# Optimization experiments

Measured on AMD Instinct MI355X. Metric: run time of the kernel, lower is better.

The kernel has to match this reference:

```python
import jax, jax.numpy as jnp
import numpy as np

SAMPLES = 16        # samples per spatial dim -> M = SAMPLES**2 sample points
SAMPLE_PAD = 0
K = 9               # nearest neighbors == conv kernel size == stride


def setup_inputs() -> dict:
    key = jax.random.key(0)
    k1, k2, k3 = jax.random.split(key, 3)
    B, C, H, W = 16, 128, 64, 64
    OUT = 128
    x = jax.random.normal(k1, (B, C, H, W), dtype=jnp.float32)
    w = jax.random.normal(k2, (OUT, C, K), dtype=jnp.float32) * 0.05
    b = jax.random.normal(k3, (OUT,), dtype=jnp.float32) * 0.05
    return {"x": x, "w": w, "b": b}


def reference(x, w, b):
    B, C, H, W = x.shape
    N = H * W
    # --- spatial sample grid (static, shape-derived) ---
    xi = jnp.round(jnp.linspace(SAMPLE_PAD, H - SAMPLE_PAD - 1, SAMPLES)).astype(jnp.int32)
    yi = jnp.round(jnp.linspace(SAMPLE_PAD, W - SAMPLE_PAD - 1, SAMPLES)).astype(jnp.int32)
    xg, yg = jnp.meshgrid(xi, yi, indexing='ij')
    x_sample = x[:, :, xg, yg].reshape(B, C, -1)          # (B, C, M)
    x1 = x.reshape(B, C, N)                                # (B, C, N)
    # --- squared Euclidean distance between tokens and samples ---
    dots = jnp.einsum('bcn,bcm->bnm', x1, x_sample)        # (B, N, M)
    n2 = jnp.sum(x1 * x1, axis=1)                          # (B, N)
    m2 = jnp.sum(x_sample * x_sample, axis=1)              # (B, M)
    dist2 = n2[:, :, None] + m2[:, None, :] - 2.0 * dots   # (B, N, M)
    # K nearest samples per token (smallest distance)
    _, idx = jax.lax.top_k(-dist2, K)                      # (B, N, K) int32
    # gather neighbor features from the sample set: (B, C, N, K)
    nbrs = jnp.take_along_axis(x_sample[:, :, None, :],
                               idx[:, None, :, :], axis=3)
    # Conv1d(kernel=K, stride=K) over the (B, C, N*K) prime tensor
    out = jnp.einsum('bcnk,ock->bon', nbrs, w) + b[None, :, None]
    return out.reshape(B, w.shape[0], H, W)
```

## Files before the change

kernel.cpp:

```cpp
#include <hip/hip_runtime.h>

#define NB   16
#define NC   128
#define NN   4096
#define NM   256
#define NK   9
#define NO   128

typedef __attribute__((ext_vector_type(8))) short bf16x8;
typedef __attribute__((ext_vector_type(4))) float f32x4;

__device__ __constant__ int d_grid16[16] = {0,4,8,13,17,21,25,29,34,38,42,46,50,55,59,63};

__device__ inline unsigned short bf16_rne(float v) {
    unsigned u = __float_as_uint(v);
    return (unsigned short)((u + 0x7FFFu + ((u >> 16) & 1u)) >> 16);
}

__device__ inline void merge16(unsigned* s, const unsigned* q) {
    unsigned r[16];
    #pragma unroll
    for (int i = 0; i < 16; ++i) r[i] = min(s[i], q[15 - i]);
    #pragma unroll
    for (int d = 8; d >= 1; d >>= 1)
        #pragma unroll
        for (int i = 0; i < 16; ++i)
            if (!(i & d)) { unsigned a = r[i], b2 = r[i + d]; r[i] = min(a, b2); r[i + d] = max(a, b2); }
    #pragma unroll
    for (int i = 0; i < 16; ++i) s[i] = r[i];
}

__global__ __launch_bounds__(256) void k_prep(const float* __restrict__ x,
                                              const float* __restrict__ w,
                                              float* __restrict__ xsT,
                                              unsigned short* __restrict__ xsTh,
                                              unsigned short* __restrict__ xsTl,
                                              unsigned short* __restrict__ Wth,
                                              unsigned short* __restrict__ Wtl,
                                              float* __restrict__ n2g,
                                              float* __restrict__ m2) {
    __shared__ float tile[16 * 260];
    int bx = blockIdx.x, t = threadIdx.x;
    if (bx < 128) {
        int b = bx >> 3, c0 = (bx & 7) * 16;
        int m = t;
        int pix = d_grid16[m >> 4] * 64 + d_grid16[m & 15];
        #pragma unroll
        for (int cc = 0; cc < 16; ++cc)
            tile[cc * 260 + m] = x[((size_t)b * NC + c0 + cc) * NN + pix];
        __syncthreads();
        #pragma unroll
        for (int e = 0; e < 4; ++e) {
            float fv[4];
            fv[0] = tile[(4 * e + 0) * 260 + m];
            fv[1] = tile[(4 * e + 1) * 260 + m];
            fv[2] = tile[(4 * e + 2) * 260 + m];
            fv[3] = tile[(4 * e + 3) * 260 + m];
            size_t base = ((size_t)b * NM + m) * NC + c0 + 4 * e;
            *(float4*)&xsT[base] = make_float4(fv[0], fv[1], fv[2], fv[3]);
            unsigned short h4[4], l4[4];
            #pragma unroll
            for (int e2 = 0; e2 < 4; ++e2) {
                unsigned short h = bf16_rne(fv[e2]);
                h4[e2] = h;
                l4[e2] = bf16_rne(fv[e2] - __uint_as_float(((unsigned)h) << 16));
            }
            *(ushort4*)&xsTh[base] = make_ushort4(h4[0], h4[1], h4[2], h4[3]);
            *(ushort4*)&xsTl[base] = make_ushort4(l4[0], l4[1], l4[2], l4[3]);
        }
    } else if (bx < 704) {
        int f = (bx - 128) * 256 + t;
        int ko = f >> 7, c = f & 127;
        int o = ko & 127, k = ko >> 7;
        float v = w[(size_t)o * 1152 + c * 9 + k];
        unsigned short h = bf16_rne(v);
        Wth[f] = h;
        Wtl[f] = bf16_rne(v - __uint_as_float(((unsigned)h) << 16));
    } else if (bx < 960) {
        #pragma clang fp contract(off)
        int i = bx - 704;
        int b = i >> 4, n = (i & 15) * 256 + t;
        const float* p = x + (size_t)b * NC * NN + n;
        float a = 0.f;
        #pragma unroll 16
        for (int c = 0; c < NC; ++c) { float v = p[(size_t)c * NN]; a = __fadd_rn(a, __fmul_rn(v, v)); }
        n2g[(size_t)b * NN + n] = a;
    } else {
        #pragma clang fp contract(off)
        int b = bx - 960;
        int pix = d_grid16[t >> 4] * 64 + d_grid16[t & 15];
        const float* p = x + (size_t)b * NC * NN + pix;
        float a = 0.f;
        #pragma unroll 16
        for (int c = 0; c < NC; ++c) { float v = p[(size_t)c * NN]; a = __fadd_rn(a, __fmul_rn(v, v)); }
        m2[b * NM + t] = a;
    }
}

__global__ __launch_bounds__(256) void k_g(const unsigned short* __restrict__ xsTh,
                                           const unsigned short* __restrict__ xsTl,
                                           const unsigned short* __restrict__ Wth,
                                           const unsigned short* __restrict__ Wtl,
                                           float* __restrict__ G) {
    int id = blockIdx.x;
    int b = id & 15, r = id >> 4;
    int kk = r % 9, mt = r / 9;
    int t = threadIdx.x;
    int w = t >> 6, lane = t & 63;
    int lr = lane & 15, quad = lane >> 4;
    int m = b * NM + mt * 64 + w * 16 + lr;
    const unsigned short* aph = xsTh + (size_t)m * NC;
    const unsigned short* apl = xsTl + (size_t)m * NC;
    f32x4 acc[8];
    #pragma unroll
    for (int j = 0; j < 8; ++j) acc[j] = (f32x4){0.f, 0.f, 0.f, 0.f};
    #pragma unroll
    for (int kb = 0; kb < 4; ++kb) {
        int co = kb * 32 + quad * 8;
        bf16x8 Ah = *(const bf16x8*)&aph[co];
        bf16x8 Al = *(const bf16x8*)&apl[co];
        #pragma unroll
        for (int j = 0; j < 8; ++j) {
            size_t wrow = ((size_t)kk * 128 + 16 * j + lr) * NC + co;
            bf16x8 Bh = *(const bf16x8*)&Wth[wrow];
            bf16x8 Bl = *(const bf16x8*)&Wtl[wrow];
            acc[j] = __builtin_amdgcn_mfma_f32_16x16x32_bf16(Ah, Bh, acc[j], 0, 0, 0);
            acc[j] = __builtin_amdgcn_mfma_f32_16x16x32_bf16(Al, Bh, acc[j], 0, 0, 0);
            acc[j] = __builtin_amdgcn_mfma_f32_16x16x32_bf16(Ah, Bl, acc[j], 0, 0, 0);
        }
    }
    int mrow = b * NM + mt * 64 + w * 16 + quad * 4;
    #pragma unroll
    for (int j = 0; j < 8; ++j)
        #pragma unroll
        for (int r2 = 0; r2 < 4; ++r2)
            G[((size_t)(mrow + r2)) * 1152 + kk * 128 + 16 * j + lr] = acc[j][r2];
}

__global__ __launch_bounds__(256, 2) void k_selref(const float* __restrict__ x,
                                                   const unsigned short* __restrict__ xsTh,
                                                   const unsigned short* __restrict__ xsTl,
                                                   const float* __restrict__ xsT,
                                                   const float* __restrict__ m2,
                                                   const float* __restrict__ n2g,
                                                   int* __restrict__ idx) {
    #pragma clang fp contract(off)
    __shared__ __align__(16) unsigned char ubuf[17408];
    __shared__ __align__(16) unsigned mrg[1088];
    __shared__ unsigned short candl[32 * 16];
    __shared__ float m2l[256];
    __shared__ float n2l[32];
    unsigned short* xhp = (unsigned short*)ubuf;
    unsigned short* xlp = xhp + 32 * 136;
    float* xr = (float*)ubuf;
    unsigned* wl = mrg;
    unsigned long long* pairs = (unsigned long long*)mrg;

    int b = blockIdx.x & 15, n0 = (blockIdx.x >> 4) * 32;
    int t = threadIdx.x;
    int w = t >> 6, lane = t & 63;
    int lr = lane & 15, quad = lane >> 4;

    m2l[t] = m2[b * NM + t];
    if (t < 32) n2l[t] = n2g[(size_t)b * NN + n0 + t];

    #pragma unroll
    for (int it = 0; it < 4; ++it) {
        int f4 = it * 256 + t;
        int c = f4 >> 3, nn4 = (f4 & 7) * 4;
        float4 v = *(const float4*)&x[((size_t)b * NC + c) * NN + n0 + nn4];
        float vf[4] = {v.x, v.y, v.z, v.w};
        #pragma unroll
        for (int e = 0; e < 4; ++e) {
            unsigned short h = bf16_rne(vf[e]);
            unsigned short l = bf16_rne(vf[e] - __uint_as_float(((unsigned)h) << 16));
            xhp[(nn4 + e) * 136 + c] = h;
            xlp[(nn4 + e) * 136 + c] = l;
        }
    }
    __syncthreads();

    f32x4 acc[2][4];
    #pragma unroll
    for (int i = 0; i < 2; ++i)
        #pragma unroll
        for (int j = 0; j < 4; ++j) acc[i][j] = (f32x4){0.f, 0.f, 0.f, 0.f};
    int mbase = w * 64;
    #pragma unroll
    for (int kb = 0; kb < 4; ++kb) {
        int co = kb * 32 + quad * 8;
        bf16x8 Bh0 = *(const bf16x8*)&xhp[lr * 136 + co];
        bf16x8 Bl0 = *(const bf16x8*)&xlp[lr * 136 + co];
        bf16x8 Bh1 = *(const bf16x8*)&xhp[(16 + lr) * 136 + co];
        bf16x8 Bl1 = *(const bf16x8*)&xlp[(16 + lr) * 136 + co];
        bf16x8 Ah[4], Al[4];
        #pragma unroll
        for (int j = 0; j < 4; ++j) {
            size_t arow = ((size_t)(b * NM + mbase + 16 * j + lr)) * NC + co;
            Ah[j] = *(const bf16x8*)&xsTh[arow];
            Al[j] = *(const bf16x8*)&xsTl[arow];
        }
        #pragma unroll
        for (int j = 0; j < 4; ++j) {
            acc[0][j] = __builtin_amdgcn_mfma_f32_16x16x32_bf16(Ah[j], Bh0, acc[0][j], 0, 0, 0);
            acc[0][j] = __builtin_amdgcn_mfma_f32_16x16x32_bf16(Ah[j], Bl0, acc[0][j], 0, 0, 0);
            acc[0][j] = __builtin_amdgcn_mfma_f32_16x16x32_bf16(Al[j], Bh0, acc[0][j], 0, 0, 0);
            acc[1][j] = __builtin_amdgcn_mfma_f32_16x16x32_bf16(Ah[j], Bh1, acc[1][j], 0, 0, 0);
            acc[1][j] = __builtin_amdgcn_mfma_f32_16x16x32_bf16(Ah[j], Bl1, acc[1][j], 0, 0, 0);
            acc[1][j] = __builtin_amdgcn_mfma_f32_16x16x32_bf16(Al[j], Bh1, acc[1][j], 0, 0, 0);
        }
    }

    #pragma unroll
    for (int h = 0; h < 2; ++h) {
        unsigned s16v[16];
        #pragma unroll
        for (int j = 0; j < 4; ++j)
            #pragma unroll
            for (int r = 0; r < 4; ++r) {
                int m = mbase + 16 * j + quad * 4 + r;
                float key = fmaf(-2.f, acc[h][j][r], m2l[m]);
                unsigned u = __float_as_uint(key);
                u = (u & 0x80000000u) ? ~u : (u | 0x80000000u);
                s16v[4 * j + r] = (u & 0xFFFFFF00u) | (unsigned)m;
            }
        #define CE(i,jx) { unsigned a_ = s16v[i], b_ = s16v[jx]; s16v[i] = min(a_, b_); s16v[jx] = max(a_, b_); }
        CE(0,1) CE(2,3) CE(0,2) CE(1,3) CE(1,2)
        CE(4,5) CE(6,7) CE(4,6) CE(5,7) CE(5,6)
        CE(0,4) CE(2,6) CE(2,4) CE(1,5) CE(3,7) CE(3,5) CE(1,2) CE(3,4) CE(5,6)
        CE(8,9) CE(10,11) CE(8,10) CE(9,11) CE(9,10)
        CE(12,13) CE(14,15) CE(12,14) CE(13,15) CE(13,14)
        CE(8,12) CE(10,14) CE(10,12) CE(9,13) CE(11,15) CE(11,13) CE(9,10) CE(11,12) CE(13,14)
        CE(0,8) CE(4,12) CE(4,8) CE(2,10) CE(6,14) CE(6,10) CE(2,4) CE(6,8) CE(10,12)
        CE(1,9) CE(5,13) CE(5,9) CE(3,11) CE(7,15) CE(7,11) CE(3,5) CE(7,9) CE(11,13)
        CE(1,2) CE(3,4) CE(5,6) CE(7,8) CE(9,10) CE(11,12) CE(13,14)
        #undef CE

        #pragma unroll
        for (int d = 16; d <= 32; d <<= 1) {
            unsigned q[16];
            #pragma unroll
            for (int i = 0; i < 16; ++i) q[i] = (unsigned)__shfl_xor((int)s16v[i], d, 64);
            merge16(s16v, q);
        }

        if (quad == 0) {
            #pragma unroll
            for (int ii = 0; ii < 4; ++ii)
                *(uint4*)&wl[(w * 16 + lr) * 16 + 4 * ii] =
                    make_uint4(s16v[4*ii], s16v[4*ii+1], s16v[4*ii+2], s16v[4*ii+3]);
        }
        __syncthreads();
        if (w == 0) {
            #pragma unroll
            for (int p = 1; p < 4; ++p) {
                unsigned q[16];
                #pragma unroll
                for (int i = 0; i < 16; ++i) q[i] = wl[(p * 16 + lr) * 16 + i];
                merge16(s16v, q);
            }
            if (quad == 0) {
                unsigned* c32 = (unsigned*)candl;
                #pragma unroll
                for (int i = 0; i < 16; i += 2)
                    c32[(16 * h + lr) * 8 + (i >> 1)] =
                        (s16v[i] & 255u) | ((s16v[i + 1] & 255u) << 16);
            }
        }
        __syncthreads();
    }

    #pragma unroll
    for (int it = 0; it < 4; ++it) {
        int f4 = it * 256 + t;
        int c = f4 >> 3, nn4 = (f4 & 7) * 4;
        float4 v = *(const float4*)&x[((size_t)b * NC + c) * NN + n0 + nn4];
        xr[(nn4 + 0) * 132 + c] = v.x;
        xr[(nn4 + 1) * 132 + c] = v.y;
        xr[(nn4 + 2) * 132 + c] = v.z;
        xr[(nn4 + 3) * 132 + c] = v.w;
    }
    __syncthreads();

    {
        int tok = t >> 3, q8 = t & 7;
        float n2 = n2l[tok];
        int mym[2];
        unsigned long long myp[2];
        #pragma unroll
        for (int s = 0; s < 2; ++s) {
            int m = candl[tok * 16 + q8 + 8 * s];
            mym[s] = m;
            const float* xt = xsT + ((size_t)(b * NM + m)) * NC;
            float dot = 0.f;
            for (int c4 = 0; c4 < 32; ++c4) {
                float4 xv = *(const float4*)&xr[tok * 132 + 4 * c4];
                float4 sv = *(const float4*)&xt[4 * c4];
                dot = __fadd_rn(dot, __fmul_rn(xv.x, sv.x));
                dot = __fadd_rn(dot, __fmul_rn(xv.y, sv.y));
                dot = __fadd_rn(dot, __fmul_rn(xv.z, sv.z));
                dot = __fadd_rn(dot, __fmul_rn(xv.w, sv.w));
            }
            float key = __fsub_rn(__fadd_rn(n2, m2l[m]), __fmul_rn(2.f, dot));
            unsigned u = __float_as_uint(key);
            u = (u & 0x80000000u) ? ~u : (u | 0x80000000u);
            myp[s] = ((unsigned long long)u << 32) | (unsigned)m;
            pairs[tok * 17 + q8 + 8 * s] = myp[s];
        }
        __syncthreads();
        unsigned long long pl[16];
        #pragma unroll
        for (int l2 = 0; l2 < 16; ++l2) pl[l2] = pairs[tok * 17 + l2];
        size_t obase = (size_t)(b * NN + n0 + tok) * NK;
        #pragma unroll
        for (int s = 0; s < 2; ++s) {
            int rank = 0;
            #pragma unroll
            for (int l2 = 0; l2 < 16; ++l2) rank += (pl[l2] < myp[s]);
            if (rank < 9) idx[obase + rank] = mym[s];
        }
    }
}

__global__ __launch_bounds__(256) void k_out(const float* __restrict__ G,
                                             const int* __restrict__ idx,
                                             const float* __restrict__ bias,
                                             float* __restrict__ out) {
    __shared__ float S[64 * 129];
    __shared__ int   idxl[576];
    __shared__ float biasl[128];
    int b = blockIdx.x & 15, n0 = (blockIdx.x >> 4) * 64;
    int t = threadIdx.x;
    if (t < 128) biasl[t] = bias[t];
    for (int f = t; f < 576; f += 256) idxl[f] = idx[(size_t)(b * NN + n0) * NK + f];
    __syncthreads();
    int o = t & 127, half = t >> 7;
    for (int p = 0; p < 32; ++p) {
        int n = p * 2 + half;
        float a = biasl[o];
        #pragma unroll
        for (int k = 0; k < 9; ++k) {
            int m = idxl[n * 9 + k];
            a += G[(((size_t)(b * NM + m)) * NK + k) * 128 + o];
        }
        S[n * 129 + o] = a;
    }
    __syncthreads();
    int nn = t & 63, ob = t >> 6;
    for (int p = 0; p < 32; ++p) {
        int o2 = p * 4 + ob;
        out[((size_t)(b * NO + o2)) * NN + n0 + nn] = S[nn * 129 + o2];
    }
}

extern "C" void kernel_launch(void* const* d_in, const int* in_sizes, int n_in,
                              void* d_out, int out_size, void* d_ws, size_t ws_size,
                              hipStream_t stream) {
    const float* x    = (const float*)d_in[0];
    const float* w    = (const float*)d_in[1];
    const float* bias = (const float*)d_in[2];
    float* out = (float*)d_out;

    float* ws   = (float*)d_ws;
    float* m2   = ws;
    float* n2g  = ws + 4096;
    float* xsT  = ws + 69632;
    float* G    = ws + 593920;
    int*   idx  = (int*)(ws + 5312512);
    unsigned short* xsTh = (unsigned short*)(ws + 5902336);
    unsigned short* xsTl = (unsigned short*)(ws + 6164480);
    unsigned short* Wth  = (unsigned short*)(ws + 6426624);
    unsigned short* Wtl  = (unsigned short*)(ws + 6500352);

    k_prep  <<<dim3(976),  dim3(256), 0, stream>>>(x, w, xsT, xsTh, xsTl, Wth, Wtl, n2g, m2);
    k_g     <<<dim3(576),  dim3(256), 0, stream>>>(xsTh, xsTl, Wth, Wtl, G);
    k_selref<<<dim3(2048), dim3(256), 0, stream>>>(x, xsTh, xsTl, xsT, m2, n2g, idx);
    k_out   <<<dim3(1024), dim3(256), 0, stream>>>(G, idx, bias, out);
}
```

Baseline: 231.2 us.

## Split fused select/refine kernel, parallelize per-half merges, halve k_g tiles

The fused select-and-refine kernel becomes two kernels. k_sel merges both token halves in parallel on waves 0 and 1 with a single barrier, and packs the 16 byte-sized candidate indices into the idx buffer. k_ref then rereads those candidates and does the exact fp32 distance refinement and ranking. k_g splits each output-channel block in half, doubling the grid and halving per-thread accumulators. The goal is fewer barriers and less serialized merging, higher occupancy and lower register pressure, at the cost of an extra launch, reloading x, and a global round trip for the candidates.

```diff
diff --git a/kernel.cpp b/kernel.cpp
--- a/kernel.cpp
+++ b/kernel.cpp
@@ -104,24 +104,25 @@
                                            float* __restrict__ G) {
     int id = blockIdx.x;
     int b = id & 15, r = id >> 4;
-    int kk = r % 9, mt = r / 9;
+    int kk = r % 9, q = r / 9;
+    int mt = q >> 1, jh = q & 1;
     int t = threadIdx.x;
     int w = t >> 6, lane = t & 63;
     int lr = lane & 15, quad = lane >> 4;
     int m = b * NM + mt * 64 + w * 16 + lr;
     const unsigned short* aph = xsTh + (size_t)m * NC;
     const unsigned short* apl = xsTl + (size_t)m * NC;
-    f32x4 acc[8];
-    #pragma unroll
-    for (int j = 0; j < 8; ++j) acc[j] = (f32x4){0.f, 0.f, 0.f, 0.f};
+    f32x4 acc[4];
+    #pragma unroll
+    for (int j = 0; j < 4; ++j) acc[j] = (f32x4){0.f, 0.f, 0.f, 0.f};
     #pragma unroll
     for (int kb = 0; kb < 4; ++kb) {
         int co = kb * 32 + quad * 8;
         bf16x8 Ah = *(const bf16x8*)&aph[co];
         bf16x8 Al = *(const bf16x8*)&apl[co];
         #pragma unroll
-        for (int j = 0; j < 8; ++j) {
-            size_t wrow = ((size_t)kk * 128 + 16 * j + lr) * NC + co;
+        for (int j = 0; j < 4; ++j) {
+            size_t wrow = ((size_t)kk * 128 + jh * 64 + 16 * j + lr) * NC + co;
             bf16x8 Bh = *(const bf16x8*)&Wth[wrow];
             bf16x8 Bl = *(const bf16x8*)&Wtl[wrow];
             acc[j] = __builtin_amdgcn_mfma_f32_16x16x32_bf16(Ah, Bh, acc[j], 0, 0, 0);
@@ -131,30 +132,21 @@
     }
     int mrow = b * NM + mt * 64 + w * 16 + quad * 4;
     #pragma unroll
-    for (int j = 0; j < 8; ++j)
+    for (int j = 0; j < 4; ++j)
         #pragma unroll
         for (int r2 = 0; r2 < 4; ++r2)
-            G[((size_t)(mrow + r2)) * 1152 + kk * 128 + 16 * j + lr] = acc[j][r2];
-}
-
-__global__ __launch_bounds__(256, 2) void k_selref(const float* __restrict__ x,
-                                                   const unsigned short* __restrict__ xsTh,
-                                                   const unsigned short* __restrict__ xsTl,
-                                                   const float* __restrict__ xsT,
-                                                   const float* __restrict__ m2,
-                                                   const float* __restrict__ n2g,
-                                                   int* __restrict__ idx) {
-    #pragma clang fp contract(off)
-    __shared__ __align__(16) unsigned char ubuf[17408];
-    __shared__ __align__(16) unsigned mrg[1088];
-    __shared__ unsigned short candl[32 * 16];
+            G[((size_t)(mrow + r2)) * 1152 + kk * 128 + jh * 64 + 16 * j + lr] = acc[j][r2];
+}
+
+__global__ __launch_bounds__(256, 2) void k_sel(const float* __restrict__ x,
+                                                const unsigned short* __restrict__ xsTh,
+                                                const unsigned short* __restrict__ xsTl,
+                                                const float* __restrict__ m2,
+                                                int* __restrict__ idx) {
+    __shared__ __align__(16) unsigned short xhp[32 * 136];
+    __shared__ __align__(16) unsigned short xlp[32 * 136];
+    __shared__ __align__(16) unsigned wl[2 * 4 * 16 * 16];
     __shared__ float m2l[256];
-    __shared__ float n2l[32];
-    unsigned short* xhp = (unsigned short*)ubuf;
-    unsigned short* xlp = xhp + 32 * 136;
-    float* xr = (float*)ubuf;
-    unsigned* wl = mrg;
-    unsigned long long* pairs = (unsigned long long*)mrg;
 
     int b = blockIdx.x & 15, n0 = (blockIdx.x >> 4) * 32;
     int t = threadIdx.x;
@@ -162,7 +154,6 @@
     int lr = lane & 15, quad = lane >> 4;
 
     m2l[t] = m2[b * NM + t];
-    if (t < 32) n2l[t] = n2g[(size_t)b * NN + n0 + t];
 
     #pragma unroll
     for (int it = 0; it < 4; ++it) {
@@ -211,9 +202,11 @@
         }
     }
 
-    #pragma unroll
-    for (int h = 0; h < 2; ++h) {
-        unsigned s16v[16];
+    unsigned s16v[16];
+    int hfirst = 1 - (w & 1);
+    #pragma unroll
+    for (int hh = 0; hh < 2; ++hh) {
+        int h = (hh == 0) ? hfirst : 1 - hfirst;
         #pragma unroll
         for (int j = 0; j < 4; ++j)
             #pragma unroll
@@ -243,32 +236,55 @@
             for (int i = 0; i < 16; ++i) q[i] = (unsigned)__shfl_xor((int)s16v[i], d, 64);
             merge16(s16v, q);
         }
-
         if (quad == 0) {
             #pragma unroll
             for (int ii = 0; ii < 4; ++ii)
-                *(uint4*)&wl[(w * 16 + lr) * 16 + 4 * ii] =
+                *(uint4*)&wl[(((h * 4 + w) * 16 + lr) * 16) + 4 * ii] =
                     make_uint4(s16v[4*ii], s16v[4*ii+1], s16v[4*ii+2], s16v[4*ii+3]);
         }
-        __syncthreads();
-        if (w == 0) {
-            #pragma unroll
-            for (int p = 1; p < 4; ++p) {
-                unsigned q[16];
-                #pragma unroll
-                for (int i = 0; i < 16; ++i) q[i] = wl[(p * 16 + lr) * 16 + i];
-                merge16(s16v, q);
-            }
-            if (quad == 0) {
-                unsigned* c32 = (unsigned*)candl;
-                #pragma unroll
-                for (int i = 0; i < 16; i += 2)
-                    c32[(16 * h + lr) * 8 + (i >> 1)] =
-                        (s16v[i] & 255u) | ((s16v[i + 1] & 255u) << 16);
-            }
-        }
-        __syncthreads();
-    }
+    }
+    __syncthreads();
+
+    if (w < 2) {
+        int h = w;
+        #pragma unroll
+        for (int p = 1; p < 4; ++p) {
+            int pw = (w + p) & 3;
+            unsigned q[16];
+            #pragma unroll
+            for (int i = 0; i < 16; ++i) q[i] = wl[(((h * 4 + pw) * 16 + lr) * 16) + i];
+            merge16(s16v, q);
+        }
+        if (quad == 0) {
+            int tok = 16 * h + lr;
+            size_t obase = (size_t)(b * NN + n0 + tok) * NK;
+            #pragma unroll
+            for (int i = 0; i < 4; ++i)
+                idx[obase + i] = (int)((s16v[4*i] & 255u) | ((s16v[4*i+1] & 255u) << 8) |
+                                       ((s16v[4*i+2] & 255u) << 16) | ((s16v[4*i+3] & 255u) << 24));
+        }
+    }
+}
+
+__global__ __launch_bounds__(256, 2) void k_ref(const float* __restrict__ x,
+                                                const float* __restrict__ xsT,
+                                                const float* __restrict__ m2,
+                                                const float* __restrict__ n2g,
+                                                int* __restrict__ idx) {
+    #pragma clang fp contract(off)
+    __shared__ __align__(16) float xr[32 * 132];
+    __shared__ unsigned long long pairs[32 * 17];
+    __shared__ unsigned char candl[512];
+    __shared__ float m2l[256];
+    __shared__ float n2l[32];
+
+    int b = blockIdx.x & 15, n0 = (blockIdx.x >> 4) * 32;
+    int t = threadIdx.x;
+
+    m2l[t] = m2[b * NM + t];
+    if (t < 32) n2l[t] = n2g[(size_t)b * NN + n0 + t];
+    if (t < 128) ((unsigned*)candl)[t] =
+        (unsigned)idx[(size_t)(b * NN + n0 + (t >> 2)) * NK + (t & 3)];
 
     #pragma unroll
     for (int it = 0; it < 4; ++it) {
@@ -282,43 +298,41 @@
     }
     __syncthreads();
 
-    {
-        int tok = t >> 3, q8 = t & 7;
-        float n2 = n2l[tok];
-        int mym[2];
-        unsigned long long myp[2];
-        #pragma unroll
-        for (int s = 0; s < 2; ++s) {
-            int m = candl[tok * 16 + q8 + 8 * s];
-            mym[s] = m;
-            const float* xt = xsT + ((size_t)(b * NM + m)) * NC;
-            float dot = 0.f;
-            for (int c4 = 0; c4 < 32; ++c4) {
-                float4 xv = *(const float4*)&xr[tok * 132 + 4 * c4];
-                float4 sv = *(const float4*)&xt[4 * c4];
-                dot = __fadd_rn(dot, __fmul_rn(xv.x, sv.x));
-                dot = __fadd_rn(dot, __fmul_rn(xv.y, sv.y));
-                dot = __fadd_rn(dot, __fmul_rn(xv.z, sv.z));
-                dot = __fadd_rn(dot, __fmul_rn(xv.w, sv.w));
-            }
-            float key = __fsub_rn(__fadd_rn(n2, m2l[m]), __fmul_rn(2.f, dot));
-            unsigned u = __float_as_uint(key);
-            u = (u & 0x80000000u) ? ~u : (u | 0x80000000u);
-            myp[s] = ((unsigned long long)u << 32) | (unsigned)m;
-            pairs[tok * 17 + q8 + 8 * s] = myp[s];
-        }
-        __syncthreads();
-        unsigned long long pl[16];
-        #pragma unroll
-        for (int l2 = 0; l2 < 16; ++l2) pl[l2] = pairs[tok * 17 + l2];
-        size_t obase = (size_t)(b * NN + n0 + tok) * NK;
-        #pragma unroll
-        for (int s = 0; s < 2; ++s) {
-            int rank = 0;
-            #pragma unroll
-            for (int l2 = 0; l2 < 16; ++l2) rank += (pl[l2] < myp[s]);
-            if (rank < 9) idx[obase + rank] = mym[s];
-        }
+    int tok = t >> 3, q8 = t & 7;
+    float n2 = n2l[tok];
+    int mym[2];
+    unsigned long long myp[2];
+    #pragma unroll
+    for (int s = 0; s < 2; ++s) {
+        int m = candl[tok * 16 + q8 + 8 * s];
+        mym[s] = m;
+        const float* xt = xsT + ((size_t)(b * NM + m)) * NC;
+        float dot = 0.f;
+        for (int c4 = 0; c4 < 32; ++c4) {
+            float4 xv = *(const float4*)&xr[tok * 132 + 4 * c4];
+            float4 sv = *(const float4*)&xt[4 * c4];
+            dot = __fadd_rn(dot, __fmul_rn(xv.x, sv.x));
+            dot = __fadd_rn(dot, __fmul_rn(xv.y, sv.y));
+            dot = __fadd_rn(dot, __fmul_rn(xv.z, sv.z));
+            dot = __fadd_rn(dot, __fmul_rn(xv.w, sv.w));
+        }
+        float key = __fsub_rn(__fadd_rn(n2, m2l[m]), __fmul_rn(2.f, dot));
+        unsigned u = __float_as_uint(key);
+        u = (u & 0x80000000u) ? ~u : (u | 0x80000000u);
+        myp[s] = ((unsigned long long)u << 32) | (unsigned)m;
+        pairs[tok * 17 + q8 + 8 * s] = myp[s];
+    }
+    __syncthreads();
+    unsigned long long pl[16];
+    #pragma unroll
+    for (int l2 = 0; l2 < 16; ++l2) pl[l2] = pairs[tok * 17 + l2];
+    size_t obase = (size_t)(b * NN + n0 + tok) * NK;
+    #pragma unroll
+    for (int s = 0; s < 2; ++s) {
+        int rank = 0;
+        #pragma unroll
+        for (int l2 = 0; l2 < 16; ++l2) rank += (pl[l2] < myp[s]);
+        if (rank < 9) idx[obase + rank] = mym[s];
     }
 }
 
@@ -372,8 +386,9 @@
     unsigned short* Wth  = (unsigned short*)(ws + 6426624);
     unsigned short* Wtl  = (unsigned short*)(ws + 6500352);
 
-    k_prep  <<<dim3(976),  dim3(256), 0, stream>>>(x, w, xsT, xsTh, xsTl, Wth, Wtl, n2g, m2);
-    k_g     <<<dim3(576),  dim3(256), 0, stream>>>(xsTh, xsTl, Wth, Wtl, G);
-    k_selref<<<dim3(2048), dim3(256), 0, stream>>>(x, xsTh, xsTl, xsT, m2, n2g, idx);
-    k_out   <<<dim3(1024), dim3(256), 0, stream>>>(G, idx, bias, out);
-}
+    k_prep<<<dim3(976),  dim3(256), 0, stream>>>(x, w, xsT, xsTh, xsTl, Wth, Wtl, n2g, m2);
+    k_g   <<<dim3(1152), dim3(256), 0, stream>>>(xsTh, xsTl, Wth, Wtl, G);
+    k_sel <<<dim3(2048), dim3(256), 0, stream>>>(x, xsTh, xsTl, m2, idx);
+    k_ref <<<dim3(2048), dim3(256), 0, stream>>>(x, xsT, m2, n2g, idx);
+    k_out <<<dim3(1024), dim3(256), 0, stream>>>(G, idx, bias, out);
+}
```

Result: slower. 260.7 us (+12.8%).

## Stage sample tiles through shared memory in selection kernel and split G kernel

Applied to the files above, without the earlier changes.

The selection kernel now streams the sample set through shared memory in 32-row tiles, loading the next tile into registers while the current one is used. Each wave computes distances for 16 tokens against 16 samples per tile, and the top-16 merge is restructured so pairs of waves merge through shared memory. The x tile is held in registers for reuse instead of being reloaded from global memory. The G kernel is split into twice as many blocks, each computing half of the output columns, to raise parallelism, at the cost of more barriers in the tile loop and more register pressure.

```diff
diff --git a/kernel.cpp b/kernel.cpp
--- a/kernel.cpp
+++ b/kernel.cpp
@@ -17,7 +17,21 @@
     return (unsigned short)((u + 0x7FFFu + ((u >> 16) & 1u)) >> 16);
 }
 
-__device__ inline void merge16(unsigned* s, const unsigned* q) {
+__device__ __forceinline__ void sort16(unsigned* s) {
+    #define CE(i,jx) { unsigned a_ = s[i], b_ = s[jx]; s[i] = min(a_, b_); s[jx] = max(a_, b_); }
+    CE(0,1) CE(2,3) CE(0,2) CE(1,3) CE(1,2)
+    CE(4,5) CE(6,7) CE(4,6) CE(5,7) CE(5,6)
+    CE(0,4) CE(2,6) CE(2,4) CE(1,5) CE(3,7) CE(3,5) CE(1,2) CE(3,4) CE(5,6)
+    CE(8,9) CE(10,11) CE(8,10) CE(9,11) CE(9,10)
+    CE(12,13) CE(14,15) CE(12,14) CE(13,15) CE(13,14)
+    CE(8,12) CE(10,14) CE(10,12) CE(9,13) CE(11,15) CE(11,13) CE(9,10) CE(11,12) CE(13,14)
+    CE(0,8) CE(4,12) CE(4,8) CE(2,10) CE(6,14) CE(6,10) CE(2,4) CE(6,8) CE(10,12)
+    CE(1,9) CE(5,13) CE(5,9) CE(3,11) CE(7,15) CE(7,11) CE(3,5) CE(7,9) CE(11,13)
+    CE(1,2) CE(3,4) CE(5,6) CE(7,8) CE(9,10) CE(11,12) CE(13,14)
+    #undef CE
+}
+
+__device__ __forceinline__ void merge16(unsigned* s, const unsigned* q) {
     unsigned r[16];
     #pragma unroll
     for (int i = 0; i < 16; ++i) r[i] = min(s[i], q[15 - i]);
@@ -104,24 +118,25 @@
                                            float* __restrict__ G) {
     int id = blockIdx.x;
     int b = id & 15, r = id >> 4;
-    int kk = r % 9, mt = r / 9;
+    int kk = r % 9, q = r / 9;
+    int mt = q >> 1, jh = q & 1;
     int t = threadIdx.x;
     int w = t >> 6, lane = t & 63;
     int lr = lane & 15, quad = lane >> 4;
     int m = b * NM + mt * 64 + w * 16 + lr;
     const unsigned short* aph = xsTh + (size_t)m * NC;
     const unsigned short* apl = xsTl + (size_t)m * NC;
-    f32x4 acc[8];
-    #pragma unroll
-    for (int j = 0; j < 8; ++j) acc[j] = (f32x4){0.f, 0.f, 0.f, 0.f};
+    f32x4 acc[4];
+    #pragma unroll
+    for (int j = 0; j < 4; ++j) acc[j] = (f32x4){0.f, 0.f, 0.f, 0.f};
     #pragma unroll
     for (int kb = 0; kb < 4; ++kb) {
         int co = kb * 32 + quad * 8;
         bf16x8 Ah = *(const bf16x8*)&aph[co];
         bf16x8 Al = *(const bf16x8*)&apl[co];
         #pragma unroll
-        for (int j = 0; j < 8; ++j) {
-            size_t wrow = ((size_t)kk * 128 + 16 * j + lr) * NC + co;
+        for (int j = 0; j < 4; ++j) {
+            size_t wrow = ((size_t)kk * 128 + jh * 64 + 16 * j + lr) * NC + co;
             bf16x8 Bh = *(const bf16x8*)&Wth[wrow];
             bf16x8 Bl = *(const bf16x8*)&Wtl[wrow];
             acc[j] = __builtin_amdgcn_mfma_f32_16x16x32_bf16(Ah, Bh, acc[j], 0, 0, 0);
@@ -131,10 +146,10 @@
     }
     int mrow = b * NM + mt * 64 + w * 16 + quad * 4;
     #pragma unroll
-    for (int j = 0; j < 8; ++j)
+    for (int j = 0; j < 4; ++j)
         #pragma unroll
         for (int r2 = 0; r2 < 4; ++r2)
-            G[((size_t)(mrow + r2)) * 1152 + kk * 128 + 16 * j + lr] = acc[j][r2];
+            G[((size_t)(mrow + r2)) * 1152 + kk * 128 + jh * 64 + 16 * j + lr] = acc[j][r2];
 }
 
 __global__ __launch_bounds__(256, 2) void k_selref(const float* __restrict__ x,
@@ -145,140 +160,141 @@
                                                    const float* __restrict__ n2g,
                                                    int* __restrict__ idx) {
     #pragma clang fp contract(off)
-    __shared__ __align__(16) unsigned char ubuf[17408];
-    __shared__ __align__(16) unsigned mrg[1088];
-    __shared__ unsigned short candl[32 * 16];
+    __shared__ __align__(16) unsigned short tokp[2 * 32 * 136];
+    __shared__ __align__(16) unsigned char  ubuf[17408];
+    __shared__ __align__(16) unsigned       wl[1088];
     __shared__ float m2l[256];
     __shared__ float n2l[32];
-    unsigned short* xhp = (unsigned short*)ubuf;
-    unsigned short* xlp = xhp + 32 * 136;
+    __shared__ unsigned char candl[512];
+    unsigned short* smp = (unsigned short*)ubuf;
     float* xr = (float*)ubuf;
-    unsigned* wl = mrg;
-    unsigned long long* pairs = (unsigned long long*)mrg;
+    unsigned long long* pairs = (unsigned long long*)wl;
 
     int b = blockIdx.x & 15, n0 = (blockIdx.x >> 4) * 32;
     int t = threadIdx.x;
     int w = t >> 6, lane = t & 63;
     int lr = lane & 15, quad = lane >> 4;
+    int h = w >> 1, msub = w & 1;
 
     m2l[t] = m2[b * NM + t];
     if (t < 32) n2l[t] = n2g[(size_t)b * NN + n0 + t];
 
+    float4 xv[4];
     #pragma unroll
     for (int it = 0; it < 4; ++it) {
         int f4 = it * 256 + t;
         int c = f4 >> 3, nn4 = (f4 & 7) * 4;
-        float4 v = *(const float4*)&x[((size_t)b * NC + c) * NN + n0 + nn4];
-        float vf[4] = {v.x, v.y, v.z, v.w};
+        xv[it] = *(const float4*)&x[((size_t)b * NC + c) * NN + n0 + nn4];
+        float vf[4] = {xv[it].x, xv[it].y, xv[it].z, xv[it].w};
         #pragma unroll
         for (int e = 0; e < 4; ++e) {
-            unsigned short h = bf16_rne(vf[e]);
-            unsigned short l = bf16_rne(vf[e] - __uint_as_float(((unsigned)h) << 16));
-            xhp[(nn4 + e) * 136 + c] = h;
-            xlp[(nn4 + e) * 136 + c] = l;
-        }
-    }
-    __syncthreads();
-
-    f32x4 acc[2][4];
-    #pragma unroll
-    for (int i = 0; i < 2; ++i)
-        #pragma unroll
-        for (int j = 0; j < 4; ++j) acc[i][j] = (f32x4){0.f, 0.f, 0.f, 0.f};
-    int mbase = w * 64;
-    #pragma unroll
-    for (int kb = 0; kb < 4; ++kb) {
-        int co = kb * 32 + quad * 8;
-        bf16x8 Bh0 = *(const bf16x8*)&xhp[lr * 136 + co];
-        bf16x8 Bl0 = *(const bf16x8*)&xlp[lr * 136 + co];
-        bf16x8 Bh1 = *(const bf16x8*)&xhp[(16 + lr) * 136 + co];
-        bf16x8 Bl1 = *(const bf16x8*)&xlp[(16 + lr) * 136 + co];
-        bf16x8 Ah[4], Al[4];
-        #pragma unroll
-        for (int j = 0; j < 4; ++j) {
-            size_t arow = ((size_t)(b * NM + mbase + 16 * j + lr)) * NC + co;
-            Ah[j] = *(const bf16x8*)&xsTh[arow];
-            Al[j] = *(const bf16x8*)&xsTl[arow];
-        }
-        #pragma unroll
-        for (int j = 0; j < 4; ++j) {
-            acc[0][j] = __builtin_amdgcn_mfma_f32_16x16x32_bf16(Ah[j], Bh0, acc[0][j], 0, 0, 0);
-            acc[0][j] = __builtin_amdgcn_mfma_f32_16x16x32_bf16(Ah[j], Bl0, acc[0][j], 0, 0, 0);
-            acc[0][j] = __builtin_amdgcn_mfma_f32_16x16x32_bf16(Al[j], Bh0, acc[0][j], 0, 0, 0);
-            acc[1][j] = __builtin_amdgcn_mfma_f32_16x16x32_bf16(Ah[j], Bh1, acc[1][j], 0, 0, 0);
-            acc[1][j] = __builtin_amdgcn_mfma_f32_16x16x32_bf16(Ah[j], Bl1, acc[1][j], 0, 0, 0);
-            acc[1][j] = __builtin_amdgcn_mfma_f32_16x16x32_bf16(Al[j], Bh1, acc[1][j], 0, 0, 0);
-        }
-    }
-
-    #pragma unroll
-    for (int h = 0; h < 2; ++h) {
-        unsigned s16v[16];
-        #pragma unroll
-        for (int j = 0; j < 4; ++j)
-            #pragma unroll
-            for (int r = 0; r < 4; ++r) {
-                int m = mbase + 16 * j + quad * 4 + r;
-                float key = fmaf(-2.f, acc[h][j][r], m2l[m]);
-                unsigned u = __float_as_uint(key);
-                u = (u & 0x80000000u) ? ~u : (u | 0x80000000u);
-                s16v[4 * j + r] = (u & 0xFFFFFF00u) | (unsigned)m;
+            unsigned short hh = bf16_rne(vf[e]);
+            unsigned short ll = bf16_rne(vf[e] - __uint_as_float(((unsigned)hh) << 16));
+            tokp[(nn4 + e) * 136 + c] = hh;
+            tokp[4352 + (nn4 + e) * 136 + c] = ll;
+        }
+    }
+    uint4 sv[4];
+    #pragma unroll
+    for (int i = 0; i < 4; ++i) {
+        int q = i * 256 + t;
+        int pl = q >> 9, row = (q >> 4) & 31, c8 = q & 15;
+        const unsigned short* src = pl ? xsTl : xsTh;
+        sv[i] = *(const uint4*)&src[((size_t)(b * NM + row)) * NC + c8 * 8];
+    }
+    #pragma unroll
+    for (int i = 0; i < 4; ++i) {
+        int q = i * 256 + t;
+        int pl = q >> 9, row = (q >> 4) & 31, c8 = q & 15;
+        *(uint4*)&smp[pl * 4352 + row * 136 + c8 * 8] = sv[i];
+    }
+    __syncthreads();
+
+    unsigned karr[32];
+    const unsigned short* tpb_h = &tokp[(h * 16 + lr) * 136];
+    const unsigned short* tpb_l = &tokp[4352 + (h * 16 + lr) * 136];
+    #pragma unroll
+    for (int tile = 0; tile < 8; ++tile) {
+        if (tile < 7) {
+            int m0n = (tile + 1) * 32;
+            #pragma unroll
+            for (int i = 0; i < 4; ++i) {
+                int q = i * 256 + t;
+                int pl = q >> 9, row = (q >> 4) & 31, c8 = q & 15;
+                const unsigned short* src = pl ? xsTl : xsTh;
+                sv[i] = *(const uint4*)&src[((size_t)(b * NM + m0n + row)) * NC + c8 * 8];
             }
-        #define CE(i,jx) { unsigned a_ = s16v[i], b_ = s16v[jx]; s16v[i] = min(a_, b_); s16v[jx] = max(a_, b_); }
-        CE(0,1) CE(2,3) CE(0,2) CE(1,3) CE(1,2)
-        CE(4,5) CE(6,7) CE(4,6) CE(5,7) CE(5,6)
-        CE(0,4) CE(2,6) CE(2,4) CE(1,5) CE(3,7) CE(3,5) CE(1,2) CE(3,4) CE(5,6)
-        CE(8,9) CE(10,11) CE(8,10) CE(9,11) CE(9,10)
-        CE(12,13) CE(14,15) CE(12,14) CE(13,15) CE(13,14)
-        CE(8,12) CE(10,14) CE(10,12) CE(9,13) CE(11,15) CE(11,13) CE(9,10) CE(11,12) CE(13,14)
-        CE(0,8) CE(4,12) CE(4,8) CE(2,10) CE(6,14) CE(6,10) CE(2,4) CE(6,8) CE(10,12)
-        CE(1,9) CE(5,13) CE(5,9) CE(3,11) CE(7,15) CE(7,11) CE(3,5) CE(7,9) CE(11,13)
-        CE(1,2) CE(3,4) CE(5,6) CE(7,8) CE(9,10) CE(11,12) CE(13,14)
-        #undef CE
-
-        #pragma unroll
-        for (int d = 16; d <= 32; d <<= 1) {
-            unsigned q[16];
-            #pragma unroll
-            for (int i = 0; i < 16; ++i) q[i] = (unsigned)__shfl_xor((int)s16v[i], d, 64);
-            merge16(s16v, q);
-        }
-
+        }
+        f32x4 acc = (f32x4){0.f, 0.f, 0.f, 0.f};
+        #pragma unroll
+        for (int kb = 0; kb < 4; ++kb) {
+            int co = kb * 32 + quad * 8;
+            bf16x8 Ah = *(const bf16x8*)&smp[(msub * 16 + lr) * 136 + co];
+            bf16x8 Al = *(const bf16x8*)&smp[4352 + (msub * 16 + lr) * 136 + co];
+            bf16x8 Bh = *(const bf16x8*)&tpb_h[co];
+            bf16x8 Bl = *(const bf16x8*)&tpb_l[co];
+            acc = __builtin_amdgcn_mfma_f32_16x16x32_bf16(Ah, Bh, acc, 0, 0, 0);
+            acc = __builtin_amdgcn_mfma_f32_16x16x32_bf16(Ah, Bl, acc, 0, 0, 0);
+            acc = __builtin_amdgcn_mfma_f32_16x16x32_bf16(Al, Bh, acc, 0, 0, 0);
+        }
+        #pragma unroll
+        for (int r = 0; r < 4; ++r) {
+            int m = tile * 32 + msub * 16 + quad * 4 + r;
+            float key = fmaf(-2.f, acc[r], m2l[m]);
+            unsigned u = __float_as_uint(key);
+            u = (u & 0x80000000u) ? ~u : (u | 0x80000000u);
+            karr[tile * 4 + r] = (u & 0xFFFFFF00u) | (unsigned)m;
+        }
+        __syncthreads();
+        if (tile < 7) {
+            #pragma unroll
+            for (int i = 0; i < 4; ++i) {
+                int q = i * 256 + t;
+                int pl = q >> 9, row = (q >> 4) & 31, c8 = q & 15;
+                *(uint4*)&smp[pl * 4352 + row * 136 + c8 * 8] = sv[i];
+            }
+            __syncthreads();
+        }
+    }
+
+    sort16(karr);
+    sort16(karr + 16);
+    merge16(karr, karr + 16);
+    #pragma unroll
+    for (int d = 16; d <= 32; d <<= 1) {
+        unsigned q[16];
+        #pragma unroll
+        for (int i = 0; i < 16; ++i) q[i] = (unsigned)__shfl_xor((int)karr[i], d, 64);
+        merge16(karr, q);
+    }
+
+    if ((w & 1) && quad == 0) {
+        #pragma unroll
+        for (int ii = 0; ii < 4; ++ii)
+            *(uint4*)&wl[(w * 16 + lr) * 16 + 4 * ii] =
+                make_uint4(karr[4*ii], karr[4*ii+1], karr[4*ii+2], karr[4*ii+3]);
+    }
+    __syncthreads();
+    if (!(w & 1)) {
+        unsigned q[16];
+        #pragma unroll
+        for (int i = 0; i < 16; ++i) q[i] = wl[((w + 1) * 16 + lr) * 16 + i];
+        merge16(karr, q);
         if (quad == 0) {
-            #pragma unroll
-            for (int ii = 0; ii < 4; ++ii)
-                *(uint4*)&wl[(w * 16 + lr) * 16 + 4 * ii] =
-                    make_uint4(s16v[4*ii], s16v[4*ii+1], s16v[4*ii+2], s16v[4*ii+3]);
-        }
-        __syncthreads();
-        if (w == 0) {
-            #pragma unroll
-            for (int p = 1; p < 4; ++p) {
-                unsigned q[16];
-                #pragma unroll
-                for (int i = 0; i < 16; ++i) q[i] = wl[(p * 16 + lr) * 16 + i];
-                merge16(s16v, q);
-            }
-            if (quad == 0) {
-                unsigned* c32 = (unsigned*)candl;
-                #pragma unroll
-                for (int i = 0; i < 16; i += 2)
-                    c32[(16 * h + lr) * 8 + (i >> 1)] =
-                        (s16v[i] & 255u) | ((s16v[i + 1] & 255u) << 16);
-            }
-        }
-        __syncthreads();
+            int tok = h * 16 + lr;
+            #pragma unroll
+            for (int i = 0; i < 16; ++i) candl[tok * 16 + i] = (unsigned char)(karr[i] & 255u);
+        }
     }
 
     #pragma unroll
     for (int it = 0; it < 4; ++it) {
         int f4 = it * 256 + t;
         int c = f4 >> 3, nn4 = (f4 & 7) * 4;
-        float4 v = *(const float4*)&x[((size_t)b * NC + c) * NN + n0 + nn4];
-        xr[(nn4 + 0) * 132 + c] = v.x;
-        xr[(nn4 + 1) * 132 + c] = v.y;
-        xr[(nn4 + 2) * 132 + c] = v.z;
-        xr[(nn4 + 3) * 132 + c] = v.w;
+        xr[(nn4 + 0) * 132 + c] = xv[it].x;
+        xr[(nn4 + 1) * 132 + c] = xv[it].y;
+        xr[(nn4 + 2) * 132 + c] = xv[it].z;
+        xr[(nn4 + 3) * 132 + c] = xv[it].w;
     }
     __syncthreads();
 
@@ -294,12 +310,12 @@
             const float* xt = xsT + ((size_t)(b * NM + m)) * NC;
             float dot = 0.f;
             for (int c4 = 0; c4 < 32; ++c4) {
-                float4 xv = *(const float4*)&xr[tok * 132 + 4 * c4];
-                float4 sv = *(const float4*)&xt[4 * c4];
-                dot = __fadd_rn(dot, __fmul_rn(xv.x, sv.x));
-                dot = __fadd_rn(dot, __fmul_rn(xv.y, sv.y));
-                dot = __fadd_rn(dot, __fmul_rn(xv.z, sv.z));
-                dot = __fadd_rn(dot, __fmul_rn(xv.w, sv.w));
+                float4 xvv = *(const float4*)&xr[tok * 132 + 4 * c4];
+                float4 svv = *(const float4*)&xt[4 * c4];
+                dot = __fadd_rn(dot, __fmul_rn(xvv.x, svv.x));
+                dot = __fadd_rn(dot, __fmul_rn(xvv.y, svv.y));
+                dot = __fadd_rn(dot, __fmul_rn(xvv.z, svv.z));
+                dot = __fadd_rn(dot, __fmul_rn(xvv.w, svv.w));
             }
             float key = __fsub_rn(__fadd_rn(n2, m2l[m]), __fmul_rn(2.f, dot));
             unsigned u = __float_as_uint(key);
@@ -373,7 +389,7 @@
     unsigned short* Wtl  = (unsigned short*)(ws + 6500352);
 
     k_prep  <<<dim3(976),  dim3(256), 0, stream>>>(x, w, xsT, xsTh, xsTl, Wth, Wtl, n2g, m2);
-    k_g     <<<dim3(576),  dim3(256), 0, stream>>>(xsTh, xsTl, Wth, Wtl, G);
+    k_g     <<<dim3(1152), dim3(256), 0, stream>>>(xsTh, xsTl, Wth, Wtl, G);
     k_selref<<<dim3(2048), dim3(256), 0, stream>>>(x, xsTh, xsTl, xsT, m2, n2g, idx);
     k_out   <<<dim3(1024), dim3(256), 0, stream>>>(G, idx, bias, out);
 }
```

Result: slower. 264.6 us (+14.5%).
